# Kernel tuning notes

Measured on AMD Instinct MI355X. Metric: run time of the kernel, lower is better.

Reference implementation:

```python
import jax, jax.numpy as jnp
import numpy as np

EMBED_DIM = 1024
NUM_HEADS = 16
D_K = EMBED_DIM // NUM_HEADS


def setup_inputs() -> dict:
    key = jax.random.key(0)
    kx, kq, kk, kv, ko = jax.random.split(key, 5)
    scale = 1.0 / np.sqrt(EMBED_DIM)
    return {
        "x": jax.random.normal(kx, (4, 2048, EMBED_DIM), dtype=jnp.float32),
        # nn.Linear weights are [out, in]; we store them the same way.
        "w_q": jax.random.normal(kq, (EMBED_DIM, EMBED_DIM), dtype=jnp.float32) * scale,
        "w_k": jax.random.normal(kk, (EMBED_DIM, EMBED_DIM), dtype=jnp.float32) * scale,
        "w_v": jax.random.normal(kv, (EMBED_DIM, EMBED_DIM), dtype=jnp.float32) * scale,
        "w_o": jax.random.normal(ko, (EMBED_DIM, EMBED_DIM), dtype=jnp.float32) * scale,
    }


def reference(x, w_q, w_k, w_v, w_o):
    B, S, E = x.shape
    H, Dk = NUM_HEADS, D_K

    def proj(w):  # [B,S,E] @ [E,E]^T -> [B,H,S,Dk]
        y = jnp.einsum('bse,fe->bsf', x, w)
        return y.reshape(B, S, H, Dk).transpose(0, 2, 1, 3)

    q, k, v = proj(w_q), proj(w_k), proj(w_v)
    scores = jnp.einsum('bhsd,bhtd->bhst', q, k) / jnp.sqrt(jnp.float32(Dk))
    attn = jax.nn.softmax(scores, axis=-1)  # dropout p=0 -> identity
    out = jnp.einsum('bhst,bhtd->bhsd', attn, v)
    out = out.transpose(0, 2, 1, 3).reshape(B, S, E)
    return jnp.einsum('bse,fe->bsf', out, w_o)
```

## Files before the change

kernel.cpp:

```cpp
#include <hip/hip_runtime.h>
#include <stdint.h>

typedef unsigned short u16;
typedef __attribute__((ext_vector_type(8))) short bf16x8;
typedef __attribute__((ext_vector_type(4))) float f32x4;
typedef __attribute__((ext_vector_type(16))) float f32x16;

#define EMB 1024
#define SLEN 2048
#define NHD 16
#define DKH 64

__device__ __forceinline__ u16 f2bf(float f) {
  uint32_t u = __float_as_uint(f);
  u = (u + 0x7fffu + ((u >> 16) & 1u)) >> 16;
  return (u16)u;
}

__device__ __forceinline__ void load_lds16(const void* g, void* l) {
  __builtin_amdgcn_global_load_lds(
      (const __attribute__((address_space(1))) uint32_t*)g,
      (__attribute__((address_space(3))) uint32_t*)l, 16, 0, 0);
}

__global__ __launch_bounds__(256) void cvt_all(
    const float* __restrict__ x,
    const float* __restrict__ w0, const float* __restrict__ w1,
    const float* __restrict__ w2, const float* __restrict__ w3,
    u16* __restrict__ xo,
    u16* __restrict__ o0, u16* __restrict__ o1,
    u16* __restrict__ o2, u16* __restrict__ o3) {
  const int bid = blockIdx.x;
  const float* in;
  u16* out;
  int i;
  if (bid < 8192) {
    in = x; out = xo; i = bid * 256 + threadIdx.x;
  } else {
    const int ws = (bid - 8192) >> 10;
    in  = (ws == 0) ? w0 : (ws == 1) ? w1 : (ws == 2) ? w2 : w3;
    out = (ws == 0) ? o0 : (ws == 1) ? o1 : (ws == 2) ? o2 : o3;
    i = ((bid - 8192) & 1023) * 256 + threadIdx.x;
  }
  float4 v = ((const float4*)in)[i];
  union { u16 h[4]; uint64_t q; } o;
  o.h[0] = f2bf(v.x); o.h[1] = f2bf(v.y); o.h[2] = f2bf(v.z); o.h[3] = f2bf(v.w);
  ((uint64_t*)out)[i] = o.q;
}

template<int MODE>
__device__ __forceinline__ void gemm_body(const u16* __restrict__ A,
                                          const u16* __restrict__ W,
                                          void* __restrict__ C,
                                          int bm, int bn,
                                          u16* At, u16* Bt) {
  const int tid = threadIdx.x;
  const int l = tid & 63, w = tid >> 6;
  const int wm = w >> 1, wn = w & 1;
  const int lr = l & 15, lg = l >> 4;

  f32x4 acc[4][4] = {};

  const int e0 = w * 1024 + l * 8;
  const int r0 = e0 >> 5, c0 = e0 & 31;
  const int e1 = e0 + 512;
  const int r1 = e1 >> 5, c1 = e1 & 31;
  const u16* Ag0 = A + (size_t)(bm + r0) * EMB + c0;
  const u16* Ag1 = A + (size_t)(bm + r1) * EMB + c1;
  const u16* Wg0 = W + (size_t)(bn + r0) * EMB + c0;
  const u16* Wg1 = W + (size_t)(bn + r1) * EMB + c1;

  auto stage = [&](int buf, int k0) {
    load_lds16(Ag0 + k0, At + buf * 4096 + w * 1024);
    load_lds16(Ag1 + k0, At + buf * 4096 + w * 1024 + 512);
    load_lds16(Wg0 + k0, Bt + buf * 4096 + w * 1024);
    load_lds16(Wg1 + k0, Bt + buf * 4096 + w * 1024 + 512);
  };

  stage(0, 0);
  stage(1, 32);
  int cur = 0;

#pragma unroll 1
  for (int it = 0; it < 32; ++it) {
    if (it < 31)
      asm volatile("s_waitcnt vmcnt(4)" ::: "memory");
    else
      asm volatile("s_waitcnt vmcnt(0)" ::: "memory");
    __builtin_amdgcn_s_barrier();
    if (it < 30) {
      int nb = cur + 2; if (nb >= 3) nb -= 3;
      stage(nb, (it + 2) * 32);
    }
    bf16x8 af[4], bf[4];
#pragma unroll
    for (int i = 0; i < 4; ++i)
      af[i] = *(const bf16x8*)(At + cur * 4096 + (wm * 64 + i * 16 + lr) * 32 + lg * 8);
#pragma unroll
    for (int j = 0; j < 4; ++j)
      bf[j] = *(const bf16x8*)(Bt + cur * 4096 + (wn * 64 + j * 16 + lr) * 32 + lg * 8);
    __builtin_amdgcn_s_setprio(1);
#pragma unroll
    for (int i = 0; i < 4; ++i)
#pragma unroll
      for (int j = 0; j < 4; ++j)
        acc[i][j] = __builtin_amdgcn_mfma_f32_16x16x32_bf16(af[i], bf[j], acc[i][j], 0, 0, 0);
    __builtin_amdgcn_s_setprio(0);
    ++cur; if (cur == 3) cur = 0;
  }

  if (MODE == 2) {
#pragma unroll
    for (int i = 0; i < 4; ++i) {
      const int m0 = bm + wm * 64 + i * 16 + lg * 4;
      const int bb = m0 >> 11;
      const int ss = m0 & 2047;
#pragma unroll
      for (int j = 0; j < 4; ++j) {
        const int n = bn + wn * 64 + j * 16 + lr;
        const int hh = n >> 6, dd = n & 63;
        union { u16 h[4]; uint64_t q; } pk;
#pragma unroll
        for (int r = 0; r < 4; ++r) pk.h[r] = f2bf(acc[i][j][r]);
        *(uint64_t*)((u16*)C + ((size_t)((bb * 16 + hh) * 64 + dd)) * 2048 + ss) = pk.q;
      }
    }
  } else {
#pragma unroll
    for (int i = 0; i < 4; ++i) {
      const int mb = bm + wm * 64 + i * 16 + lg * 4;
#pragma unroll
      for (int j = 0; j < 4; ++j) {
        const int col = bn + wn * 64 + j * 16 + lr;
#pragma unroll
        for (int r = 0; r < 4; ++r) {
          float v = acc[i][j][r];
          if (MODE == 1) v *= 0.18033688011112042f;
          if (MODE == 3)
            ((float*)C)[(size_t)(mb + r) * EMB + col] = v;
          else
            ((u16*)C)[(size_t)(mb + r) * EMB + col] = f2bf(v);
        }
      }
    }
  }
}

__global__ __launch_bounds__(256) void gemm_qkv(
    const u16* __restrict__ A,
    const u16* __restrict__ wq, const u16* __restrict__ wk, const u16* __restrict__ wv,
    u16* __restrict__ Qo, u16* __restrict__ Ko, u16* __restrict__ Vo) {
  __shared__ __align__(16) u16 At[3 * 4096];
  __shared__ __align__(16) u16 Bt[3 * 4096];
  const int bid = blockIdx.x;
  const int wgid = (bid & 7) * 192 + (bid >> 3);
  const int z = wgid >> 9;
  const int rem = wgid & 511;
  const int bm = (rem >> 3) * 128, bn = (rem & 7) * 128;
  if (z == 0) gemm_body<1>(A, wq, Qo, bm, bn, At, Bt);
  else if (z == 1) gemm_body<0>(A, wk, Ko, bm, bn, At, Bt);
  else gemm_body<2>(A, wv, Vo, bm, bn, At, Bt);
}

__global__ __launch_bounds__(256) void gemm_out(const u16* __restrict__ A,
                                                const u16* __restrict__ W,
                                                float* __restrict__ C) {
  __shared__ __align__(16) u16 At[3 * 4096];
  __shared__ __align__(16) u16 Bt[3 * 4096];
  const int bid = blockIdx.x;
  const int wgid = (bid & 7) * 64 + (bid >> 3);
  const int bm = (wgid >> 3) * 128, bn = (wgid & 7) * 128;
  gemm_body<3>(A, W, C, bm, bn, At, Bt);
}

__global__ __launch_bounds__(512, 4) void attn_fwd(const u16* __restrict__ Q,
                                                   const u16* __restrict__ K,
                                                   const u16* __restrict__ VT,
                                                   u16* __restrict__ O) {
  __shared__ __align__(16) u16 lds[3][2][64 * 64];
  const int tid = threadIdx.x;
  const int l = tid & 63, w = tid >> 6;
  const int ql = l & 31, hi = l >> 5;
  const int bid = blockIdx.x;
  const int bh = (bid & 7) * 8 + (bid >> 6);
  const int qt = (bid >> 3) & 7;
  const int b = bh >> 4, h = bh & 15;
  const int qw = qt * 256 + w * 32;
  const size_t qkb = ((size_t)b * SLEN) * EMB + h * DKH;
  const size_t vb = (size_t)bh * DKH * SLEN;

  const int srow = tid >> 3;
  const int scb = ((tid & 7) * 16) ^ ((srow & 7) << 4);
  const u16* Ksrc = K + qkb + (size_t)srow * EMB + (scb >> 1);
  const u16* Vsrc = VT + vb + (size_t)srow * SLEN + (scb >> 1);

  auto stage = [&](int buf, int t) {
    load_lds16(Ksrc + (size_t)t * 64 * EMB, (char*)(&lds[buf][0][0]) + w * 1024);
    load_lds16(Vsrc + t * 64, (char*)(&lds[buf][1][0]) + w * 1024);
  };

  bf16x8 qf[4];
#pragma unroll
  for (int ks = 0; ks < 4; ++ks)
    qf[ks] = *(const bf16x8*)(Q + qkb + (size_t)(qw + ql) * EMB + ks * 16 + hi * 8);

  f32x16 accd[2] = {};
  float lsum = 0.f;

  stage(0, 0);
  stage(1, 1);
  int cur = 0;
#pragma unroll 1
  for (int t = 0; t < 32; ++t) {
    if (t < 30) {
      int nb = cur + 2; if (nb >= 3) nb -= 3;
      stage(nb, t + 2);
      asm volatile("s_waitcnt vmcnt(4)" ::: "memory");
    } else if (t == 30) {
      asm volatile("s_waitcnt vmcnt(2)" ::: "memory");
    } else {
      asm volatile("s_waitcnt vmcnt(0)" ::: "memory");
    }
    __builtin_amdgcn_s_barrier();

    const u16* Kt = &lds[cur][0][0];
    const u16* Vt = &lds[cur][1][0];

    f32x16 sacc[2] = {};
    __builtin_amdgcn_s_setprio(1);
#pragma unroll
    for (int kf2 = 0; kf2 < 2; ++kf2) {
      const int row = kf2 * 32 + ql;
      const int swz = (row & 7) << 4;
#pragma unroll
      for (int ks = 0; ks < 4; ++ks) {
        bf16x8 kf = *(const bf16x8*)((const char*)Kt + row * 128 +
                                     ((ks * 32 + hi * 16) ^ swz));
        sacc[kf2] = __builtin_amdgcn_mfma_f32_32x32x16_bf16(kf, qf[ks], sacc[kf2], 0, 0, 0);
      }
    }
    __builtin_amdgcn_s_setprio(0);

#pragma unroll
    for (int kf2 = 0; kf2 < 2; ++kf2)
#pragma unroll
      for (int r = 0; r < 16; ++r)
        sacc[kf2][r] = __builtin_amdgcn_exp2f(sacc[kf2][r]);
    float ps[8];
#pragma unroll
    for (int g = 0; g < 8; ++g) {
      const int kf2 = g >> 2, r0 = (g & 3) * 4;
      ps[g] = (sacc[kf2][r0] + sacc[kf2][r0 + 1]) + (sacc[kf2][r0 + 2] + sacc[kf2][r0 + 3]);
    }
    lsum += ((ps[0] + ps[1]) + (ps[2] + ps[3])) + ((ps[4] + ps[5]) + (ps[6] + ps[7]));

    __builtin_amdgcn_s_setprio(1);
#pragma unroll
    for (int ks = 0; ks < 4; ++ks) {
      const int kf2 = ks >> 1;
      const int e0 = (ks & 1) * 8;
      uint32_t a0, a1, b0, b1;
      asm("v_cvt_pk_bf16_f32 %0, %1, %2" : "=v"(a0) : "v"(sacc[kf2][e0 + 0]), "v"(sacc[kf2][e0 + 1]));
      asm("v_cvt_pk_bf16_f32 %0, %1, %2" : "=v"(a1) : "v"(sacc[kf2][e0 + 2]), "v"(sacc[kf2][e0 + 3]));
      asm("v_cvt_pk_bf16_f32 %0, %1, %2" : "=v"(b0) : "v"(sacc[kf2][e0 + 4]), "v"(sacc[kf2][e0 + 5]));
      asm("v_cvt_pk_bf16_f32 %0, %1, %2" : "=v"(b1) : "v"(sacc[kf2][e0 + 6]), "v"(sacc[kf2][e0 + 7]));
      asm("v_permlane32_swap_b32 %0, %1" : "+v"(a0), "+v"(b0));
      asm("v_permlane32_swap_b32 %0, %1" : "+v"(a1), "+v"(b1));
      union { uint32_t d[4]; bf16x8 v; } pa;
      pa.d[0] = a0; pa.d[1] = a1; pa.d[2] = b0; pa.d[3] = b1;
#pragma unroll
      for (int df = 0; df < 2; ++df) {
        const int vr = df * 32 + ql;
        bf16x8 vf = *(const bf16x8*)((const char*)Vt + vr * 128 +
                                     ((ks * 32 + hi * 16) ^ ((vr & 7) << 4)));
        accd[df] = __builtin_amdgcn_mfma_f32_32x32x16_bf16(pa.v, vf, accd[df], 0, 0, 0);
      }
    }
    __builtin_amdgcn_s_setprio(0);
    __builtin_amdgcn_s_barrier();
    ++cur; if (cur == 3) cur = 0;
  }

  lsum += __shfl_xor(lsum, 32, 64);

  __syncthreads();
  u16* slice = &lds[0][0][0] + w * 2048;
#pragma unroll
  for (int reg = 0; reg < 16; ++reg) {
    const int rowq = (reg & 3) + 8 * (reg >> 2) + 4 * hi;
    const float li = 1.0f / __shfl(lsum, rowq, 64);
    slice[rowq * 64 + ql] = f2bf(accd[0][reg] * li);
    slice[rowq * 64 + 32 + ql] = f2bf(accd[1][reg] * li);
  }
  asm volatile("s_waitcnt lgkmcnt(0)" ::: "memory");
#pragma unroll
  for (int j = 0; j < 4; ++j) {
    const int byteoff = j * 1024 + l * 16;
    const int row = byteoff >> 7;
    const int colB = byteoff & 127;
    bf16x8 vv = *(const bf16x8*)((const char*)slice + byteoff);
    *(bf16x8*)(O + qkb + (size_t)(qw + row) * EMB + (colB >> 1)) = vv;
  }
}

extern "C" void kernel_launch(void* const* d_in, const int* in_sizes, int n_in,
                              void* d_out, int out_size, void* d_ws, size_t ws_size,
                              hipStream_t stream) {
  const float* x  = (const float*)d_in[0];
  const float* wq = (const float*)d_in[1];
  const float* wk = (const float*)d_in[2];
  const float* wv = (const float*)d_in[3];
  const float* wo = (const float*)d_in[4];

  char* ws = (char*)d_ws;
  u16* xb  = (u16*)(ws + 0);
  u16* wqb = (u16*)(ws + 16777216);
  u16* wkb = (u16*)(ws + 18874368);
  u16* wvb = (u16*)(ws + 20971520);
  u16* wob = (u16*)(ws + 23068672);
  u16* Qb  = (u16*)(ws + 25165824);
  u16* Kb  = (u16*)(ws + 41943040);
  u16* VTb = (u16*)(ws + 58720256);
  u16* AO  = (u16*)(ws + 75497472);

  cvt_all<<<dim3(12288), 256, 0, stream>>>(x, wq, wk, wv, wo, xb, wqb, wkb, wvb, wob);

  gemm_qkv<<<dim3(1536), 256, 0, stream>>>(xb, wqb, wkb, wvb, Qb, Kb, VTb);
  attn_fwd<<<dim3(512), 512, 0, stream>>>(Qb, Kb, VTb, AO);
  gemm_out<<<dim3(512), 256, 0, stream>>>(AO, wob, (float*)d_out);
}
```

Baseline: 176.6 us.

## Use 256x256 tiles with 8 waves and phased double-buffered staging for QKV GEMM

Replaces the 128x128, 4-wave QKV projection GEMM with a 256x256 tile per 512-thread block. K is split into 64-wide steps, double-buffered in 128KB of LDS, and the next tile's loads are interleaved across four compute phases. The larger tile halves the global and LDS traffic per FLOP and cuts the grid from 1536 to 384 blocks. In exchange, occupancy drops (large LDS use, 128 accumulator floats per lane) and there are more barriers per K step. The output GEMM is split into its own specialized body.

```diff
diff --git a/kernel.cpp b/kernel.cpp
--- a/kernel.cpp
+++ b/kernel.cpp
@@ -49,11 +49,132 @@
 }
 
 template<int MODE>
-__device__ __forceinline__ void gemm_body(const u16* __restrict__ A,
-                                          const u16* __restrict__ W,
-                                          void* __restrict__ C,
-                                          int bm, int bn,
-                                          u16* At, u16* Bt) {
+__device__ __forceinline__ void gemm256_body(const u16* __restrict__ A,
+                                             const u16* __restrict__ W,
+                                             void* __restrict__ C,
+                                             int bm, int bn, u16* L) {
+  const int tid = threadIdx.x;
+  const int l = tid & 63, w = tid >> 6;
+  const int wm = w >> 2, wn = w & 3;
+  const int lr = l & 15, lg = l >> 4;
+
+  f32x4 acc[8][4] = {};
+
+  const int row0 = tid >> 2;
+  const int g8 = (tid & 3) * 8;
+  const u16* Asrc = A + (size_t)(bm + row0) * EMB + g8;
+  const u16* Wsrc = W + (size_t)(bn + row0) * EMB + g8;
+  const int dst0 = w * 1024 + l * 16;
+
+  auto stageA = [&](int buf, int kt, int kh) {
+    char* hb = (char*)L + (size_t)(buf * 32768 + kh * 8192) * 2;
+    const u16* s = Asrc + kt * 64 + kh * 32;
+    load_lds16(s, hb + dst0);
+    load_lds16(s + (size_t)128 * EMB, hb + 8192 + dst0);
+  };
+  auto stageB = [&](int buf, int kt, int kh) {
+    char* hb = (char*)L + (size_t)(buf * 32768 + 16384 + kh * 8192) * 2;
+    const u16* s = Wsrc + kt * 64 + kh * 32;
+    load_lds16(s, hb + dst0);
+    load_lds16(s + (size_t)128 * EMB, hb + 8192 + dst0);
+  };
+
+  stageA(0, 0, 0); stageA(0, 0, 1); stageB(0, 0, 0); stageB(0, 0, 1);
+  stageA(1, 1, 0); stageB(1, 1, 0);
+  asm volatile("s_waitcnt vmcnt(4)" ::: "memory");
+  __builtin_amdgcn_s_barrier();
+
+#pragma unroll 1
+  for (int kt = 0; kt < 16; ++kt) {
+    const int buf = kt & 1;
+    const u16* Ab = L + buf * 32768;
+    const u16* Bb = L + buf * 32768 + 16384;
+#pragma unroll
+    for (int ph = 0; ph < 4; ++ph) {
+      const int kh = ph >> 1, nh = ph & 1;
+      bf16x8 af[8], bf[2];
+#pragma unroll
+      for (int i = 0; i < 8; ++i)
+        af[i] = *(const bf16x8*)(Ab + kh * 8192 + (wm * 128 + i * 16 + lr) * 32 + lg * 8);
+#pragma unroll
+      for (int j = 0; j < 2; ++j)
+        bf[j] = *(const bf16x8*)(Bb + kh * 8192 + (wn * 64 + nh * 32 + j * 16 + lr) * 32 + lg * 8);
+      if (ph == 0)      { if (kt < 15) stageA(buf ^ 1, kt + 1, 1); }
+      else if (ph == 1) { if (kt < 15) stageB(buf ^ 1, kt + 1, 1); }
+      else if (ph == 2) { if (kt < 14) stageA(buf, kt + 2, 0); }
+      else              { if (kt < 14) stageB(buf, kt + 2, 0); }
+      __builtin_amdgcn_s_barrier();
+      asm volatile("s_waitcnt lgkmcnt(0)" ::: "memory");
+      __builtin_amdgcn_s_setprio(1);
+#pragma unroll
+      for (int i = 0; i < 8; ++i)
+#pragma unroll
+        for (int j = 0; j < 2; ++j)
+          acc[i][nh * 2 + j] = __builtin_amdgcn_mfma_f32_16x16x32_bf16(
+              af[i], bf[j], acc[i][nh * 2 + j], 0, 0, 0);
+      __builtin_amdgcn_s_setprio(0);
+      if (ph == 3) {
+        if (kt < 14) asm volatile("s_waitcnt vmcnt(4)" ::: "memory");
+        else         asm volatile("s_waitcnt vmcnt(0)" ::: "memory");
+      }
+      __builtin_amdgcn_s_barrier();
+    }
+  }
+
+  if (MODE == 2) {
+#pragma unroll
+    for (int i = 0; i < 8; ++i) {
+      const int m0 = bm + wm * 128 + i * 16 + lg * 4;
+      const int bb = m0 >> 11;
+      const int ss = m0 & 2047;
+#pragma unroll
+      for (int c = 0; c < 4; ++c) {
+        const int n = bn + wn * 64 + c * 16 + lr;
+        const int hh = n >> 6, dd = n & 63;
+        union { u16 h[4]; uint64_t q; } pk;
+#pragma unroll
+        for (int r = 0; r < 4; ++r) pk.h[r] = f2bf(acc[i][c][r]);
+        *(uint64_t*)((u16*)C + ((size_t)((bb * 16 + hh) * 64 + dd)) * 2048 + ss) = pk.q;
+      }
+    }
+  } else {
+#pragma unroll
+    for (int i = 0; i < 8; ++i) {
+      const int mb = bm + wm * 128 + i * 16 + lg * 4;
+#pragma unroll
+      for (int c = 0; c < 4; ++c) {
+        const int col = bn + wn * 64 + c * 16 + lr;
+#pragma unroll
+        for (int r = 0; r < 4; ++r) {
+          float v = acc[i][c][r];
+          if (MODE == 1) v *= 0.18033688011112042f;
+          ((u16*)C)[(size_t)(mb + r) * EMB + col] = f2bf(v);
+        }
+      }
+    }
+  }
+}
+
+__global__ __launch_bounds__(512, 2) void gemm_qkv(
+    const u16* __restrict__ A,
+    const u16* __restrict__ wq, const u16* __restrict__ wk, const u16* __restrict__ wv,
+    u16* __restrict__ Qo, u16* __restrict__ Ko, u16* __restrict__ Vo) {
+  __shared__ __align__(16) u16 L[65536];
+  const int bid = blockIdx.x;
+  const int wgid = (bid & 7) * 48 + (bid >> 3);
+  const int z = wgid >> 7;
+  const int rem = wgid & 127;
+  const int bm = (rem >> 2) * 256, bn = (rem & 3) * 256;
+  if (z == 0) gemm256_body<1>(A, wq, Qo, bm, bn, L);
+  else if (z == 1) gemm256_body<0>(A, wk, Ko, bm, bn, L);
+  else gemm256_body<2>(A, wv, Vo, bm, bn, L);
+}
+
+__device__ __forceinline__ void gemm_body_out(const u16* __restrict__ A,
+                                              const u16* __restrict__ W,
+                                              float* __restrict__ C,
+                                              int bm, int bn,
+                                              u16* At, u16* Bt) {
   const int tid = threadIdx.x;
   const int l = tid & 63, w = tid >> 6;
   const int wm = w >> 1, wn = w & 1;
@@ -109,57 +230,17 @@
     ++cur; if (cur == 3) cur = 0;
   }
 
-  if (MODE == 2) {
-#pragma unroll
-    for (int i = 0; i < 4; ++i) {
-      const int m0 = bm + wm * 64 + i * 16 + lg * 4;
-      const int bb = m0 >> 11;
-      const int ss = m0 & 2047;
-#pragma unroll
-      for (int j = 0; j < 4; ++j) {
-        const int n = bn + wn * 64 + j * 16 + lr;
-        const int hh = n >> 6, dd = n & 63;
-        union { u16 h[4]; uint64_t q; } pk;
-#pragma unroll
-        for (int r = 0; r < 4; ++r) pk.h[r] = f2bf(acc[i][j][r]);
-        *(uint64_t*)((u16*)C + ((size_t)((bb * 16 + hh) * 64 + dd)) * 2048 + ss) = pk.q;
-      }
-    }
-  } else {
-#pragma unroll
-    for (int i = 0; i < 4; ++i) {
-      const int mb = bm + wm * 64 + i * 16 + lg * 4;
-#pragma unroll
-      for (int j = 0; j < 4; ++j) {
-        const int col = bn + wn * 64 + j * 16 + lr;
-#pragma unroll
-        for (int r = 0; r < 4; ++r) {
-          float v = acc[i][j][r];
-          if (MODE == 1) v *= 0.18033688011112042f;
-          if (MODE == 3)
-            ((float*)C)[(size_t)(mb + r) * EMB + col] = v;
-          else
-            ((u16*)C)[(size_t)(mb + r) * EMB + col] = f2bf(v);
-        }
-      }
-    }
-  }
-}
-
-__global__ __launch_bounds__(256) void gemm_qkv(
-    const u16* __restrict__ A,
-    const u16* __restrict__ wq, const u16* __restrict__ wk, const u16* __restrict__ wv,
-    u16* __restrict__ Qo, u16* __restrict__ Ko, u16* __restrict__ Vo) {
-  __shared__ __align__(16) u16 At[3 * 4096];
-  __shared__ __align__(16) u16 Bt[3 * 4096];
-  const int bid = blockIdx.x;
-  const int wgid = (bid & 7) * 192 + (bid >> 3);
-  const int z = wgid >> 9;
-  const int rem = wgid & 511;
-  const int bm = (rem >> 3) * 128, bn = (rem & 7) * 128;
-  if (z == 0) gemm_body<1>(A, wq, Qo, bm, bn, At, Bt);
-  else if (z == 1) gemm_body<0>(A, wk, Ko, bm, bn, At, Bt);
-  else gemm_body<2>(A, wv, Vo, bm, bn, At, Bt);
+#pragma unroll
+  for (int i = 0; i < 4; ++i) {
+    const int mb = bm + wm * 64 + i * 16 + lg * 4;
+#pragma unroll
+    for (int j = 0; j < 4; ++j) {
+      const int col = bn + wn * 64 + j * 16 + lr;
+#pragma unroll
+      for (int r = 0; r < 4; ++r)
+        C[(size_t)(mb + r) * EMB + col] = acc[i][j][r];
+    }
+  }
 }
 
 __global__ __launch_bounds__(256) void gemm_out(const u16* __restrict__ A,
@@ -170,7 +251,7 @@
   const int bid = blockIdx.x;
   const int wgid = (bid & 7) * 64 + (bid >> 3);
   const int bm = (wgid >> 3) * 128, bn = (wgid & 7) * 128;
-  gemm_body<3>(A, W, C, bm, bn, At, Bt);
+  gemm_body_out(A, W, C, bm, bn, At, Bt);
 }
 
 __global__ __launch_bounds__(512, 4) void attn_fwd(const u16* __restrict__ Q,
@@ -325,7 +406,7 @@
 
   cvt_all<<<dim3(12288), 256, 0, stream>>>(x, wq, wk, wv, wo, xb, wqb, wkb, wvb, wob);
 
-  gemm_qkv<<<dim3(1536), 256, 0, stream>>>(xb, wqb, wkb, wvb, Qb, Kb, VTb);
+  gemm_qkv<<<dim3(384), 512, 0, stream>>>(xb, wqb, wkb, wvb, Qb, Kb, VTb);
   attn_fwd<<<dim3(512), 512, 0, stream>>>(Qb, Kb, VTb, AO);
   gemm_out<<<dim3(512), 256, 0, stream>>>(AO, wob, (float*)d_out);
 }
```

Result: slower. 199.1 us (+12.7%).
